# Kernel tuning notes

Measured on AMD Instinct MI355X. Metric: run time of the kernel, lower is better.

## Reference

```python
import jax, jax.numpy as jnp
import numpy as np

B, S, D, H, DH, DK = 2, 2048, 1024, 16, 64, 64


def setup_inputs() -> dict:
    key = jax.random.key(0)
    ks = jax.random.split(key, 11)
    scale_in = 1.0 / np.sqrt(D)
    return {
        "Q": jax.random.normal(ks[0], (B, S, D), jnp.float32),
        "K": jax.random.normal(ks[1], (B, S, D), jnp.float32),
        "V": jax.random.normal(ks[2], (B, S, D), jnp.float32),
        "Wq": jax.random.normal(ks[3], (H, D, DH), jnp.float32) * scale_in,
        "bq": jax.random.normal(ks[4], (H, DH), jnp.float32) * 0.02,
        "Wk": jax.random.normal(ks[5], (H, D, DH), jnp.float32) * scale_in,
        "bk": jax.random.normal(ks[6], (H, DH), jnp.float32) * 0.02,
        "Wv": jax.random.normal(ks[7], (H, D, DH), jnp.float32) * scale_in,
        "bv": jax.random.normal(ks[8], (H, DH), jnp.float32) * 0.02,
        "Wf": jax.random.normal(ks[9], (D, D), jnp.float32) * scale_in,
        "bf": jax.random.normal(ks[10], (D,), jnp.float32) * 0.02,
    }


def reference(Q, K, V, Wq, bq, Wk, bk, Wv, bv, Wf, bf):
    # Per-head projections, vectorized over the head axis h. [B,H,S,DH]
    Qh = jnp.einsum("bsd,hde->bhse", Q, Wq) + bq[None, :, None, :]
    Kh = jnp.einsum("bsd,hde->bhse", K, Wk) + bk[None, :, None, :]
    Vh = jnp.einsum("bsd,hde->bhse", V, Wv) + bv[None, :, None, :]
    inv_sqrt_dk = jnp.asarray(1.0 / np.sqrt(DK), Qh.dtype)
    # Full attention matrix [B,H,S,S] (faithful to the naive original).
    scores = jnp.einsum("bhse,bhte->bhst", Qh, Kh) * inv_sqrt_dk
    attn = jax.nn.softmax(scores, axis=-1)  # F.softmax default -> last dim
    out = jnp.einsum("bhst,bhte->bhse", attn, Vh)  # [B,H,S,DH]
    # Concat heads on the feature axis: [B,S,H*DH] == [B,S,D]
    out = out.transpose(0, 2, 1, 3).reshape(Q.shape[0], Q.shape[1], -1)
    return out @ Wf + bf
```

## Files before the change

### kernel.cpp

```cpp
#include <hip/hip_runtime.h>

#define DEV __device__ __forceinline__

typedef unsigned short u16;
typedef unsigned int   u32;
typedef __attribute__((ext_vector_type(4)))  float f32x4;
typedef __attribute__((ext_vector_type(8)))  short s16x8;
typedef __attribute__((ext_vector_type(2)))  u32   u32x2;

static constexpr size_t OFF_QBF  = 0;
static constexpr size_t OFF_KBF  = 8388608;
static constexpr size_t OFF_VBF  = 16777216;
static constexpr size_t OFF_WCAT = 25165824;
static constexpr size_t OFF_WFT  = 31457280;
static constexpr size_t OFF_BIAS = 33554432;
static constexpr size_t OFF_QKVH = 33566720;
static constexpr size_t OFF_VT   = 58732544;
static constexpr size_t OFF_OBUF = 67121152;

DEV u16 f2bf(float f) {
  union { float f; u32 u; } a; a.f = f;
  u32 r = a.u + 0x7FFFu + ((a.u >> 16) & 1u);
  return (u16)(r >> 16);
}

#if __has_builtin(__builtin_amdgcn_exp2f)
DEV float fast_exp2(float x) { return __builtin_amdgcn_exp2f(x); }
#else
DEV float fast_exp2(float x) { return exp2f(x); }
#endif

DEV f32x4 mfma16(s16x8 a, s16x8 b, f32x4 c) {
  return __builtin_amdgcn_mfma_f32_16x16x32_bf16(a, b, c, 0, 0, 0);
}

DEV void gload_lds16(const void* g, void* l) {
  __builtin_amdgcn_global_load_lds(
      (__attribute__((address_space(1))) void*)g,
      (__attribute__((address_space(3))) void*)l, 16, 0, 0);
}


__global__ __launch_bounds__(256) void cvt3_k(const float* __restrict__ Q,
                                              const float* __restrict__ K,
                                              const float* __restrict__ V,
                                              u16* __restrict__ dst) {
  size_t idx = (size_t)blockIdx.x * 256 + threadIdx.x;
  size_t t   = idx >> 20;
  size_t r   = idx & 1048575;
  const float* src = (t == 0) ? Q : (t == 1) ? K : V;
  f32x4 v = *(const f32x4*)(src + r * 4);
  u32x2 o;
  o[0] = (u32)f2bf(v[0]) | ((u32)f2bf(v[1]) << 16);
  o[1] = (u32)f2bf(v[2]) | ((u32)f2bf(v[3]) << 16);
  *(u32x2*)(dst + idx * 4) = o;
}

__global__ __launch_bounds__(256) void prep_wqkv_k(const float* __restrict__ Wq,
                                                   const float* __restrict__ Wk,
                                                   const float* __restrict__ Wv,
                                                   u16* __restrict__ Wcat) {
  const int dt = blockIdx.x, h = blockIdx.y, z = blockIdx.z;
  const float* W = (z == 0) ? Wq : (z == 1) ? Wk : Wv;
  __shared__ u16 t[64][65];
#pragma unroll
  for (int p = 0; p < 16; ++p) {
    int idx = threadIdx.x + p * 256;
    int r = idx >> 6, e = idx & 63;
    t[r][e] = f2bf(W[((size_t)h * 1024 + dt * 64 + r) * 64 + e]);
  }
  __syncthreads();
#pragma unroll
  for (int p = 0; p < 16; ++p) {
    int idx = threadIdx.x + p * 256;
    int e = idx >> 6, r = idx & 63;
    Wcat[((size_t)z * 1024 + h * 64 + e) * 1024 + dt * 64 + r] = t[r][e];
  }
}

__global__ __launch_bounds__(256) void prep_wf_k(const float* __restrict__ Wf,
                                                 u16* __restrict__ WfT) {
  const int dt = blockIdx.x, ft = blockIdx.y;
  __shared__ u16 t[64][65];
#pragma unroll
  for (int p = 0; p < 16; ++p) {
    int idx = threadIdx.x + p * 256;
    int r = idx >> 6, f = idx & 63;
    t[r][f] = f2bf(Wf[(size_t)(dt * 64 + r) * 1024 + ft * 64 + f]);
  }
  __syncthreads();
#pragma unroll
  for (int p = 0; p < 16; ++p) {
    int idx = threadIdx.x + p * 256;
    int f = idx >> 6, r = idx & 63;
    WfT[(size_t)(ft * 64 + f) * 1024 + dt * 64 + r] = t[r][f];
  }
}

__global__ __launch_bounds__(256) void prep_bias_k(const float* __restrict__ bq,
                                                   const float* __restrict__ bk,
                                                   const float* __restrict__ bv,
                                                   float* __restrict__ biascat) {
  int i = blockIdx.x * 256 + threadIdx.x;
  if (i < 1024) biascat[i] = bq[i];
  else if (i < 2048) biascat[i] = bk[i - 1024];
  else if (i < 3072) biascat[i] = bv[i - 2048];
}

__global__ __launch_bounds__(256) void transpose_vh_k(const u16* __restrict__ QKVh,
                                                      u16* __restrict__ Vt) {
  const int nt = blockIdx.x, mt = blockIdx.y;
  __shared__ u16 t[64][72];
#pragma unroll
  for (int p = 0; p < 16; ++p) {
    int idx = threadIdx.x + p * 256;
    int r = idx >> 6, c = idx & 63;
    t[r][c] = QKVh[(size_t)(mt * 64 + r) * 3072 + 2048 + nt * 64 + c];
  }
  __syncthreads();
#pragma unroll
  for (int p = 0; p < 16; ++p) {
    int idx = threadIdx.x + p * 256;
    int c = idx >> 6, r = idx & 63;
    Vt[(size_t)(nt * 64 + c) * 4096 + mt * 64 + r] = t[r][c];
  }
}

template <int BF16_OUT>
DEV void gemm128(const u16* __restrict__ A, int lda,
                 const u16* __restrict__ B, int ldb,
                 const float* __restrict__ bias,
                 void* __restrict__ Cp, size_t ldc, int K) {
  __shared__ u16 Ash[128 * 32];
  __shared__ u16 Bsh[128 * 32];
  const int tid = threadIdx.x;
  const int lane = tid & 63;
  const int w = tid >> 6;
  const int wr = w >> 1, wc = w & 1;
  const int lr = lane >> 2;
  const int lc = (lane & 3) << 3;
  const int l15 = lane & 15, lg = lane >> 4;

  f32x4 acc[4][4];
#pragma unroll
  for (int i = 0; i < 4; ++i)
#pragma unroll
    for (int j = 0; j < 4; ++j) acc[i][j] = f32x4{0.f, 0.f, 0.f, 0.f};

  for (int kt = 0; kt < K; kt += 32) {
    if (kt) __syncthreads();
#pragma unroll
    for (int j = 0; j < 2; ++j) {
      const u16* ga = A + (size_t)(w * 32 + j * 16 + lr) * lda + kt + lc;
      gload_lds16(ga, (char*)Ash + (w * 2 + j) * 1024);
      const u16* gb = B + (size_t)(w * 32 + j * 16 + lr) * ldb + kt + lc;
      gload_lds16(gb, (char*)Bsh + (w * 2 + j) * 1024);
    }
    __syncthreads();
    s16x8 af[4], bv_[4];
#pragma unroll
    for (int i = 0; i < 4; ++i) {
      af[i]  = *(const s16x8*)&Ash[(wr * 64 + i * 16 + l15) * 32 + lg * 8];
      bv_[i] = *(const s16x8*)&Bsh[(wc * 64 + i * 16 + l15) * 32 + lg * 8];
    }
#pragma unroll
    for (int mf = 0; mf < 4; ++mf)
#pragma unroll
      for (int nf = 0; nf < 4; ++nf)
        acc[mf][nf] = mfma16(af[mf], bv_[nf], acc[mf][nf]);
  }
#pragma unroll
  for (int nf = 0; nf < 4; ++nf) {
    const int nn = wc * 64 + nf * 16 + l15;
    const float bvv = bias[nn];
#pragma unroll
    for (int mf = 0; mf < 4; ++mf)
#pragma unroll
      for (int j = 0; j < 4; ++j) {
        const int mm = wr * 64 + mf * 16 + lg * 4 + j;
        float v = acc[mf][nf][j] + bvv;
        if (BF16_OUT) ((u16*)Cp)[(size_t)mm * ldc + nn] = f2bf(v);
        else          ((float*)Cp)[(size_t)mm * ldc + nn] = v;
      }
  }
}

__global__ __launch_bounds__(256) void proj_gemm_k(const u16* __restrict__ Qb,
                                                   const u16* __restrict__ Kb,
                                                   const u16* __restrict__ Vb,
                                                   const u16* __restrict__ Wcat,
                                                   const float* __restrict__ biascat,
                                                   u16* __restrict__ QKVh) {
  const int z = blockIdx.z;
  const u16* A = (z == 0) ? Qb : (z == 1) ? Kb : Vb;
  const int m0 = blockIdx.y * 128;
  const int nl = blockIdx.x * 128;
  gemm128<1>(A + (size_t)m0 * 1024, 1024,
             Wcat + (size_t)(z * 1024 + nl) * 1024, 1024,
             biascat + z * 1024 + nl,
             QKVh + (size_t)m0 * 3072 + z * 1024 + nl, 3072, 1024);
}

__global__ __launch_bounds__(256) void final_gemm_k(const u16* __restrict__ Obuf,
                                                    const u16* __restrict__ WfT,
                                                    const float* __restrict__ bf,
                                                    float* __restrict__ out) {
  const int m0 = blockIdx.y * 128;
  const int n0 = blockIdx.x * 128;
  gemm128<0>(Obuf + (size_t)m0 * 1024, 1024,
             WfT + (size_t)n0 * 1024, 1024,
             bf + n0,
             out + (size_t)m0 * 1024 + n0, 1024, 1024);
}

__global__ __launch_bounds__(256) void attn4_k(const u16* __restrict__ QKVh,
                                               const u16* __restrict__ Vt,
                                               u16* __restrict__ Obuf) {
  const int id = blockIdx.x;
  const int virt = (id & 7) * 64 + (id >> 3);
  const int qb = virt & 15;
  const int hb = virt >> 4;
  const int h = hb & 15, b = hb >> 4;

  const int tid = threadIdx.x, lane = tid & 63, w = tid >> 6;
  const int l15 = lane & 15, lg = lane >> 4;

  __shared__ u16 Ksh[64 * 64];
  __shared__ u16 Vsh[64 * 64];
  __shared__ u16 Psh[4][32 * 64];

  const size_t rowQ = (size_t)(b * 2048 + qb * 128);
  const u16* Qbase = QKVh + rowQ * 3072 + h * 64;
  const u16* Kbase = QKVh + (size_t)(b * 2048) * 3072 + 1024 + h * 64;
  const u16* Vbase = Vt + (size_t)(h * 64) * 4096 + b * 2048;

  s16x8 aq[2][2];
#pragma unroll
  for (int mf = 0; mf < 2; ++mf)
#pragma unroll
    for (int kf = 0; kf < 2; ++kf)
      aq[mf][kf] = *(const s16x8*)(Qbase + (size_t)(w * 32 + mf * 16 + l15) * 3072 + kf * 32 + lg * 8);

  f32x4 accO[2][4];
  f32x4 lacc[2];
#pragma unroll
  for (int mf = 0; mf < 2; ++mf) {
#pragma unroll
    for (int nf = 0; nf < 4; ++nf) accO[mf][nf] = f32x4{0.f, 0.f, 0.f, 0.f};
    lacc[mf] = f32x4{0.f, 0.f, 0.f, 0.f};
  }

  const float CSC = 0.18033688011112042f;
  const float M2 = 12.0f;
  const s16x8 ONESV = {0x3F80, 0x3F80, 0x3F80, 0x3F80,
                       0x3F80, 0x3F80, 0x3F80, 0x3F80};

  const int sr = tid >> 3, ch = tid & 7;
  const int sswz = (sr & 7) << 4;
  const u16* Kg = Kbase + (size_t)sr * 3072 + ch * 8;
  const u16* Vg = Vbase + (size_t)sr * 4096 + ch * 8;

  s16x8 kreg0 = *(const s16x8*)Kg;
  s16x8 kreg1 = *(const s16x8*)(Kg + (size_t)32 * 3072);
  s16x8 vreg0 = *(const s16x8*)Vg;
  s16x8 vreg1 = *(const s16x8*)(Vg + (size_t)32 * 4096);
  Kg += (size_t)64 * 3072;
  Vg += 64;

  for (int kt = 0; kt < 32; ++kt) {
    if (kt) __syncthreads();
    *(s16x8*)((char*)Ksh + sr * 128 + ((ch * 16) ^ sswz)) = kreg0;
    *(s16x8*)((char*)Ksh + (sr + 32) * 128 + ((ch * 16) ^ sswz)) = kreg1;
    *(s16x8*)((char*)Vsh + sr * 128 + ((ch * 16) ^ sswz)) = vreg0;
    *(s16x8*)((char*)Vsh + (sr + 32) * 128 + ((ch * 16) ^ sswz)) = vreg1;
    __syncthreads();

    if (kt < 31) {
      kreg0 = *(const s16x8*)Kg;
      kreg1 = *(const s16x8*)(Kg + (size_t)32 * 3072);
      vreg0 = *(const s16x8*)Vg;
      vreg1 = *(const s16x8*)(Vg + (size_t)32 * 4096);
      Kg += (size_t)64 * 3072;
      Vg += 64;
    }

    f32x4 sc[2][4];
#pragma unroll
    for (int mf = 0; mf < 2; ++mf)
#pragma unroll
      for (int nf = 0; nf < 4; ++nf) sc[mf][nf] = f32x4{0.f, 0.f, 0.f, 0.f};
#pragma unroll
    for (int kf = 0; kf < 2; ++kf) {
      s16x8 kb[4];
#pragma unroll
      for (int nf = 0; nf < 4; ++nf) {
        int row = nf * 16 + l15;
        kb[nf] = *(const s16x8*)((char*)Ksh + row * 128 + ((kf * 64 + lg * 16) ^ ((row & 7) << 4)));
      }
#pragma unroll
      for (int mf = 0; mf < 2; ++mf)
#pragma unroll
        for (int nf = 0; nf < 4; ++nf)
          sc[mf][nf] = mfma16(aq[mf][kf], kb[nf], sc[mf][nf]);
    }

#pragma unroll
    for (int mf = 0; mf < 2; ++mf)
#pragma unroll
      for (int nf = 0; nf < 4; ++nf)
#pragma unroll
        for (int j = 0; j < 4; ++j)
          sc[mf][nf][j] = fast_exp2(fmaf(sc[mf][nf][j], CSC, -M2));

    char* pbase = (char*)&Psh[w][0];
#pragma unroll
    for (int mf = 0; mf < 2; ++mf)
#pragma unroll
      for (int nf = 0; nf < 4; ++nf)
#pragma unroll
        for (int j = 0; j < 4; ++j) {
          int srow = mf * 16 + lg * 4 + j;
          int tcol = nf * 16 + l15;
          *(u16*)(pbase + srow * 128 + ((tcol * 2) ^ ((srow & 7) << 4))) =
              f2bf(sc[mf][nf][j]);
        }
    asm volatile("s_waitcnt lgkmcnt(0)" ::: "memory");

#pragma unroll
    for (int kf = 0; kf < 2; ++kf) {
      s16x8 pa[2], vb[4];
#pragma unroll
      for (int mf = 0; mf < 2; ++mf) {
        int row = mf * 16 + l15;
        pa[mf] = *(const s16x8*)(pbase + row * 128 + ((kf * 64 + lg * 16) ^ ((row & 7) << 4)));
      }
#pragma unroll
      for (int nf = 0; nf < 4; ++nf) {
        int row = nf * 16 + l15;
        vb[nf] = *(const s16x8*)((char*)Vsh + row * 128 + ((kf * 64 + lg * 16) ^ ((row & 7) << 4)));
      }
#pragma unroll
      for (int mf = 0; mf < 2; ++mf) {
#pragma unroll
        for (int nf = 0; nf < 4; ++nf)
          accO[mf][nf] = mfma16(pa[mf], vb[nf], accO[mf][nf]);
        lacc[mf] = mfma16(pa[mf], ONESV, lacc[mf]);
      }
    }
  }

  u16* Ob = Obuf + rowQ * 1024 + h * 64;
  float inv[2][4];
#pragma unroll
  for (int mf = 0; mf < 2; ++mf)
#pragma unroll
    for (int j = 0; j < 4; ++j) inv[mf][j] = 1.f / lacc[mf][j];
#pragma unroll
  for (int mf = 0; mf < 2; ++mf)
#pragma unroll
    for (int nf = 0; nf < 4; ++nf)
#pragma unroll
      for (int j = 0; j < 4; ++j)
        Ob[(size_t)(w * 32 + mf * 16 + lg * 4 + j) * 1024 + nf * 16 + l15] =
            f2bf(accO[mf][nf][j] * inv[mf][j]);
}

extern "C" void kernel_launch(void* const* d_in, const int* in_sizes, int n_in,
                              void* d_out, int out_size, void* d_ws, size_t ws_size,
                              hipStream_t stream) {
  const float* Q  = (const float*)d_in[0];
  const float* K  = (const float*)d_in[1];
  const float* V  = (const float*)d_in[2];
  const float* Wq = (const float*)d_in[3];
  const float* bq = (const float*)d_in[4];
  const float* Wk = (const float*)d_in[5];
  const float* bk = (const float*)d_in[6];
  const float* Wv = (const float*)d_in[7];
  const float* bv = (const float*)d_in[8];
  const float* Wf = (const float*)d_in[9];
  const float* bf = (const float*)d_in[10];
  float* out = (float*)d_out;
  char* ws = (char*)d_ws;

  u16*   Qbf    = (u16*)(ws + OFF_QBF);
  u16*   Kbf    = (u16*)(ws + OFF_KBF);
  u16*   Vbf    = (u16*)(ws + OFF_VBF);
  u16*   Wcat   = (u16*)(ws + OFF_WCAT);
  u16*   WfT    = (u16*)(ws + OFF_WFT);
  float* biascat= (float*)(ws + OFF_BIAS);
  u16*   QKVh   = (u16*)(ws + OFF_QKVH);
  u16*   Vt     = (u16*)(ws + OFF_VT);
  u16*   Obuf   = (u16*)(ws + OFF_OBUF);

  dim3 blk(256);
  cvt3_k<<<12288, blk, 0, stream>>>(Q, K, V, Qbf);
  prep_wqkv_k<<<dim3(16, 16, 3), blk, 0, stream>>>(Wq, Wk, Wv, Wcat);
  prep_wf_k<<<dim3(16, 16), blk, 0, stream>>>(Wf, WfT);
  prep_bias_k<<<12, blk, 0, stream>>>(bq, bk, bv, biascat);
  proj_gemm_k<<<dim3(8, 32, 3), blk, 0, stream>>>(Qbf, Kbf, Vbf, Wcat, biascat, QKVh);
  transpose_vh_k<<<dim3(16, 64), blk, 0, stream>>>(QKVh, Vt);
  attn4_k<<<dim3(512), blk, 0, stream>>>(QKVh, Vt, Obuf);
  final_gemm_k<<<dim3(8, 32), blk, 0, stream>>>(Obuf, WfT, bf, out);
}
```

Baseline: 148.5 us.

## Load K/V MFMA fragments directly from global memory, dropping LDS staging and barriers

The attention kernel no longer stages K and V tiles through shared memory with block-wide barriers. Each wave now loads its MFMA operand fragments for K and V straight from global memory, relying on L1/L2 because all four waves read the same tiles. K fragments are double-buffered in registers across iterations. Launch bounds now request two blocks per CU. This removes the syncthreads and LDS traffic but quadruples global/L2 load requests and raises register pressure.

```diff
diff --git a/kernel.cpp b/kernel.cpp
--- a/kernel.cpp
+++ b/kernel.cpp
@@ -213,9 +213,9 @@
              out + (size_t)m0 * 1024 + n0, 1024, 1024);
 }
 
-__global__ __launch_bounds__(256) void attn4_k(const u16* __restrict__ QKVh,
-                                               const u16* __restrict__ Vt,
-                                               u16* __restrict__ Obuf) {
+__global__ __launch_bounds__(256, 2) void attn5_k(const u16* __restrict__ QKVh,
+                                                  const u16* __restrict__ Vt,
+                                                  u16* __restrict__ Obuf) {
   const int id = blockIdx.x;
   const int virt = (id & 7) * 64 + (id >> 3);
   const int qb = virt & 15;
@@ -225,8 +225,6 @@
   const int tid = threadIdx.x, lane = tid & 63, w = tid >> 6;
   const int l15 = lane & 15, lg = lane >> 4;
 
-  __shared__ u16 Ksh[64 * 64];
-  __shared__ u16 Vsh[64 * 64];
   __shared__ u16 Psh[4][32 * 64];
 
   const size_t rowQ = (size_t)(b * 2048 + qb * 128);
@@ -255,34 +253,26 @@
   const s16x8 ONESV = {0x3F80, 0x3F80, 0x3F80, 0x3F80,
                        0x3F80, 0x3F80, 0x3F80, 0x3F80};
 
-  const int sr = tid >> 3, ch = tid & 7;
-  const int sswz = (sr & 7) << 4;
-  const u16* Kg = Kbase + (size_t)sr * 3072 + ch * 8;
-  const u16* Vg = Vbase + (size_t)sr * 4096 + ch * 8;
-
-  s16x8 kreg0 = *(const s16x8*)Kg;
-  s16x8 kreg1 = *(const s16x8*)(Kg + (size_t)32 * 3072);
-  s16x8 vreg0 = *(const s16x8*)Vg;
-  s16x8 vreg1 = *(const s16x8*)(Vg + (size_t)32 * 4096);
-  Kg += (size_t)64 * 3072;
-  Vg += 64;
-
-  for (int kt = 0; kt < 32; ++kt) {
-    if (kt) __syncthreads();
-    *(s16x8*)((char*)Ksh + sr * 128 + ((ch * 16) ^ sswz)) = kreg0;
-    *(s16x8*)((char*)Ksh + (sr + 32) * 128 + ((ch * 16) ^ sswz)) = kreg1;
-    *(s16x8*)((char*)Vsh + sr * 128 + ((ch * 16) ^ sswz)) = vreg0;
-    *(s16x8*)((char*)Vsh + (sr + 32) * 128 + ((ch * 16) ^ sswz)) = vreg1;
-    __syncthreads();
-
-    if (kt < 31) {
-      kreg0 = *(const s16x8*)Kg;
-      kreg1 = *(const s16x8*)(Kg + (size_t)32 * 3072);
-      vreg0 = *(const s16x8*)Vg;
-      vreg1 = *(const s16x8*)(Vg + (size_t)32 * 4096);
-      Kg += (size_t)64 * 3072;
-      Vg += 64;
-    }
+  const u16* Kf = Kbase + (size_t)l15 * 3072 + lg * 8;
+  const u16* Vf = Vbase + (size_t)l15 * 4096 + lg * 8;
+  char* pbase = (char*)&Psh[w][0];
+
+  auto LOADK = [&](s16x8 (&dst)[2][4], int t) {
+#pragma unroll
+    for (int kf = 0; kf < 2; ++kf)
+#pragma unroll
+      for (int nf = 0; nf < 4; ++nf)
+        dst[kf][nf] = *(const s16x8*)(Kf + (size_t)(t * 64 + nf * 16) * 3072 + kf * 32);
+  };
+
+  auto TILE = [&](s16x8 (&kcur)[2][4], s16x8 (&knext)[2][4], int kt) {
+    if (kt + 1 < 32) LOADK(knext, kt + 1);
+    s16x8 vb[2][4];
+#pragma unroll
+    for (int kf = 0; kf < 2; ++kf)
+#pragma unroll
+      for (int nf = 0; nf < 4; ++nf)
+        vb[kf][nf] = *(const s16x8*)(Vf + (size_t)(nf * 16) * 4096 + kt * 64 + kf * 32);
 
     f32x4 sc[2][4];
 #pragma unroll
@@ -290,19 +280,12 @@
 #pragma unroll
       for (int nf = 0; nf < 4; ++nf) sc[mf][nf] = f32x4{0.f, 0.f, 0.f, 0.f};
 #pragma unroll
-    for (int kf = 0; kf < 2; ++kf) {
-      s16x8 kb[4];
-#pragma unroll
-      for (int nf = 0; nf < 4; ++nf) {
-        int row = nf * 16 + l15;
-        kb[nf] = *(const s16x8*)((char*)Ksh + row * 128 + ((kf * 64 + lg * 16) ^ ((row & 7) << 4)));
-      }
+    for (int kf = 0; kf < 2; ++kf)
 #pragma unroll
       for (int mf = 0; mf < 2; ++mf)
 #pragma unroll
         for (int nf = 0; nf < 4; ++nf)
-          sc[mf][nf] = mfma16(aq[mf][kf], kb[nf], sc[mf][nf]);
-    }
+          sc[mf][nf] = mfma16(aq[mf][kf], kcur[kf][nf], sc[mf][nf]);
 
 #pragma unroll
     for (int mf = 0; mf < 2; ++mf)
@@ -312,7 +295,6 @@
         for (int j = 0; j < 4; ++j)
           sc[mf][nf][j] = fast_exp2(fmaf(sc[mf][nf][j], CSC, -M2));
 
-    char* pbase = (char*)&Psh[w][0];
 #pragma unroll
     for (int mf = 0; mf < 2; ++mf)
 #pragma unroll
@@ -328,25 +310,27 @@
 
 #pragma unroll
     for (int kf = 0; kf < 2; ++kf) {
-      s16x8 pa[2], vb[4];
+      s16x8 pa[2];
 #pragma unroll
       for (int mf = 0; mf < 2; ++mf) {
         int row = mf * 16 + l15;
         pa[mf] = *(const s16x8*)(pbase + row * 128 + ((kf * 64 + lg * 16) ^ ((row & 7) << 4)));
       }
 #pragma unroll
-      for (int nf = 0; nf < 4; ++nf) {
-        int row = nf * 16 + l15;
-        vb[nf] = *(const s16x8*)((char*)Vsh + row * 128 + ((kf * 64 + lg * 16) ^ ((row & 7) << 4)));
-      }
-#pragma unroll
       for (int mf = 0; mf < 2; ++mf) {
 #pragma unroll
         for (int nf = 0; nf < 4; ++nf)
-          accO[mf][nf] = mfma16(pa[mf], vb[nf], accO[mf][nf]);
+          accO[mf][nf] = mfma16(pa[mf], vb[kf][nf], accO[mf][nf]);
         lacc[mf] = mfma16(pa[mf], ONESV, lacc[mf]);
       }
     }
+  };
+
+  s16x8 kbufA[2][4], kbufB[2][4];
+  LOADK(kbufA, 0);
+  for (int kt = 0; kt < 32; kt += 2) {
+    TILE(kbufA, kbufB, kt);
+    TILE(kbufB, kbufA, kt + 1);
   }
 
   u16* Ob = Obuf + rowQ * 1024 + h * 64;
@@ -399,6 +383,6 @@
   prep_bias_k<<<12, blk, 0, stream>>>(bq, bk, bv, biascat);
   proj_gemm_k<<<dim3(8, 32, 3), blk, 0, stream>>>(Qbf, Kbf, Vbf, Wcat, biascat, QKVh);
   transpose_vh_k<<<dim3(16, 64), blk, 0, stream>>>(QKVh, Vt);
-  attn4_k<<<dim3(512), blk, 0, stream>>>(QKVh, Vt, Obuf);
+  attn5_k<<<dim3(512), blk, 0, stream>>>(QKVh, Vt, Obuf);
   final_gemm_k<<<dim3(8, 32), blk, 0, stream>>>(Obuf, WfT, bf, out);
 }
```

New measurement: 209.1 us. 1.41x slower.

## Merge prep kernels into one launch and write V projection transposed

Applied to the files above, without the earlier changes.

Four preprocessing kernels (input bf16 conversion, QKV weight transpose, Wf transpose, bias concat) are merged into one launch that branches on block index. The V projection GEMM now writes its bf16 output directly in transposed layout, with packed 8-byte stores, so the separate transpose kernel and its extra pass over V are gone. A sched_barrier is added in the attention kernel after the P store wait. Together these cut launch overhead and memory traffic, but the transposed store pattern may coalesce less well than the row-major stores.

```diff
diff --git a/kernel.cpp b/kernel.cpp
--- a/kernel.cpp
+++ b/kernel.cpp
@@ -23,6 +23,9 @@
   u32 r = a.u + 0x7FFFu + ((a.u >> 16) & 1u);
   return (u16)(r >> 16);
 }
+DEV u32 f2bf2(float lo, float hi_) {
+  return (u32)f2bf(lo) | ((u32)f2bf(hi_) << 16);
+}
 
 #if __has_builtin(__builtin_amdgcn_exp2f)
 DEV float fast_exp2(float x) { return __builtin_amdgcn_exp2f(x); }
@@ -40,93 +43,74 @@
       (__attribute__((address_space(3))) void*)l, 16, 0, 0);
 }
 
-
-__global__ __launch_bounds__(256) void cvt3_k(const float* __restrict__ Q,
-                                              const float* __restrict__ K,
-                                              const float* __restrict__ V,
-                                              u16* __restrict__ dst) {
-  size_t idx = (size_t)blockIdx.x * 256 + threadIdx.x;
-  size_t t   = idx >> 20;
-  size_t r   = idx & 1048575;
-  const float* src = (t == 0) ? Q : (t == 1) ? K : V;
-  f32x4 v = *(const f32x4*)(src + r * 4);
-  u32x2 o;
-  o[0] = (u32)f2bf(v[0]) | ((u32)f2bf(v[1]) << 16);
-  o[1] = (u32)f2bf(v[2]) | ((u32)f2bf(v[3]) << 16);
-  *(u32x2*)(dst + idx * 4) = o;
-}
-
-__global__ __launch_bounds__(256) void prep_wqkv_k(const float* __restrict__ Wq,
-                                                   const float* __restrict__ Wk,
-                                                   const float* __restrict__ Wv,
-                                                   u16* __restrict__ Wcat) {
-  const int dt = blockIdx.x, h = blockIdx.y, z = blockIdx.z;
-  const float* W = (z == 0) ? Wq : (z == 1) ? Wk : Wv;
-  __shared__ u16 t[64][65];
-#pragma unroll
-  for (int p = 0; p < 16; ++p) {
-    int idx = threadIdx.x + p * 256;
-    int r = idx >> 6, e = idx & 63;
-    t[r][e] = f2bf(W[((size_t)h * 1024 + dt * 64 + r) * 64 + e]);
-  }
-  __syncthreads();
-#pragma unroll
-  for (int p = 0; p < 16; ++p) {
-    int idx = threadIdx.x + p * 256;
-    int e = idx >> 6, r = idx & 63;
-    Wcat[((size_t)z * 1024 + h * 64 + e) * 1024 + dt * 64 + r] = t[r][e];
-  }
-}
-
-__global__ __launch_bounds__(256) void prep_wf_k(const float* __restrict__ Wf,
-                                                 u16* __restrict__ WfT) {
-  const int dt = blockIdx.x, ft = blockIdx.y;
-  __shared__ u16 t[64][65];
-#pragma unroll
-  for (int p = 0; p < 16; ++p) {
-    int idx = threadIdx.x + p * 256;
-    int r = idx >> 6, f = idx & 63;
-    t[r][f] = f2bf(Wf[(size_t)(dt * 64 + r) * 1024 + ft * 64 + f]);
-  }
-  __syncthreads();
-#pragma unroll
-  for (int p = 0; p < 16; ++p) {
-    int idx = threadIdx.x + p * 256;
-    int f = idx >> 6, r = idx & 63;
-    WfT[(size_t)(ft * 64 + f) * 1024 + dt * 64 + r] = t[r][f];
-  }
-}
-
-__global__ __launch_bounds__(256) void prep_bias_k(const float* __restrict__ bq,
-                                                   const float* __restrict__ bk,
-                                                   const float* __restrict__ bv,
-                                                   float* __restrict__ biascat) {
-  int i = blockIdx.x * 256 + threadIdx.x;
-  if (i < 1024) biascat[i] = bq[i];
-  else if (i < 2048) biascat[i] = bk[i - 1024];
-  else if (i < 3072) biascat[i] = bv[i - 2048];
-}
-
-__global__ __launch_bounds__(256) void transpose_vh_k(const u16* __restrict__ QKVh,
-                                                      u16* __restrict__ Vt) {
-  const int nt = blockIdx.x, mt = blockIdx.y;
+__global__ __launch_bounds__(256) void prep_all_k(const float* __restrict__ Q,
+                                                  const float* __restrict__ K,
+                                                  const float* __restrict__ V,
+                                                  const float* __restrict__ Wq,
+                                                  const float* __restrict__ Wk,
+                                                  const float* __restrict__ Wv,
+                                                  const float* __restrict__ Wf,
+                                                  const float* __restrict__ bq,
+                                                  const float* __restrict__ bk,
+                                                  const float* __restrict__ bv,
+                                                  u16* __restrict__ QKVbf,
+                                                  u16* __restrict__ Wcat,
+                                                  u16* __restrict__ WfT,
+                                                  float* __restrict__ biascat) {
+  const int bid = blockIdx.x;
   __shared__ u16 t[64][72];
-#pragma unroll
-  for (int p = 0; p < 16; ++p) {
-    int idx = threadIdx.x + p * 256;
-    int r = idx >> 6, c = idx & 63;
-    t[r][c] = QKVh[(size_t)(mt * 64 + r) * 3072 + 2048 + nt * 64 + c];
-  }
-  __syncthreads();
-#pragma unroll
-  for (int p = 0; p < 16; ++p) {
-    int idx = threadIdx.x + p * 256;
-    int c = idx >> 6, r = idx & 63;
-    Vt[(size_t)(nt * 64 + c) * 4096 + mt * 64 + r] = t[r][c];
-  }
-}
-
-template <int BF16_OUT>
+  if (bid < 12288) {
+    size_t idx = (size_t)bid * 256 + threadIdx.x;
+    size_t tt  = idx >> 20;
+    size_t r   = idx & 1048575;
+    const float* src = (tt == 0) ? Q : (tt == 1) ? K : V;
+    f32x4 v = *(const f32x4*)(src + r * 4);
+    u32x2 o;
+    o[0] = f2bf2(v[0], v[1]);
+    o[1] = f2bf2(v[2], v[3]);
+    *(u32x2*)(QKVbf + idx * 4) = o;
+  } else if (bid < 13056) {
+    const int q = bid - 12288;
+    const int dt = q & 15, h = (q >> 4) & 15, z = q >> 8;
+    const float* W = (z == 0) ? Wq : (z == 1) ? Wk : Wv;
+#pragma unroll
+    for (int p = 0; p < 16; ++p) {
+      int idx = threadIdx.x + p * 256;
+      int r = idx >> 6, e = idx & 63;
+      t[r][e] = f2bf(W[((size_t)h * 1024 + dt * 64 + r) * 64 + e]);
+    }
+    __syncthreads();
+#pragma unroll
+    for (int p = 0; p < 16; ++p) {
+      int idx = threadIdx.x + p * 256;
+      int e = idx >> 6, r = idx & 63;
+      Wcat[((size_t)z * 1024 + h * 64 + e) * 1024 + dt * 64 + r] = t[r][e];
+    }
+  } else if (bid < 13312) {
+    const int q = bid - 13056;
+    const int dt = q & 15, ft = q >> 4;
+#pragma unroll
+    for (int p = 0; p < 16; ++p) {
+      int idx = threadIdx.x + p * 256;
+      int r = idx >> 6, f = idx & 63;
+      t[r][f] = f2bf(Wf[(size_t)(dt * 64 + r) * 1024 + ft * 64 + f]);
+    }
+    __syncthreads();
+#pragma unroll
+    for (int p = 0; p < 16; ++p) {
+      int idx = threadIdx.x + p * 256;
+      int f = idx >> 6, r = idx & 63;
+      WfT[(size_t)(ft * 64 + f) * 1024 + dt * 64 + r] = t[r][f];
+    }
+  } else {
+    int i = (bid - 13312) * 256 + threadIdx.x;
+    if (i < 1024) biascat[i] = bq[i];
+    else if (i < 2048) biascat[i] = bk[i - 1024];
+    else if (i < 3072) biascat[i] = bv[i - 2048];
+  }
+}
+
+template <int MODE>
 DEV void gemm128(const u16* __restrict__ A, int lda,
                  const u16* __restrict__ B, int ldb,
                  const float* __restrict__ bias,
@@ -174,14 +158,23 @@
     const int nn = wc * 64 + nf * 16 + l15;
     const float bvv = bias[nn];
 #pragma unroll
-    for (int mf = 0; mf < 4; ++mf)
-#pragma unroll
-      for (int j = 0; j < 4; ++j) {
-        const int mm = wr * 64 + mf * 16 + lg * 4 + j;
-        float v = acc[mf][nf][j] + bvv;
-        if (BF16_OUT) ((u16*)Cp)[(size_t)mm * ldc + nn] = f2bf(v);
-        else          ((float*)Cp)[(size_t)mm * ldc + nn] = v;
+    for (int mf = 0; mf < 4; ++mf) {
+      if (MODE == 2) {
+        const int mm0 = wr * 64 + mf * 16 + lg * 4;
+        u32x2 d;
+        d[0] = f2bf2(acc[mf][nf][0] + bvv, acc[mf][nf][1] + bvv);
+        d[1] = f2bf2(acc[mf][nf][2] + bvv, acc[mf][nf][3] + bvv);
+        *(u32x2*)((u16*)Cp + (size_t)nn * ldc + mm0) = d;
+      } else {
+#pragma unroll
+        for (int j = 0; j < 4; ++j) {
+          const int mm = wr * 64 + mf * 16 + lg * 4 + j;
+          float v = acc[mf][nf][j] + bvv;
+          if (MODE == 1) ((u16*)Cp)[(size_t)mm * ldc + nn] = f2bf(v);
+          else           ((float*)Cp)[(size_t)mm * ldc + nn] = v;
+        }
       }
+    }
   }
 }
 
@@ -190,15 +183,23 @@
                                                    const u16* __restrict__ Vb,
                                                    const u16* __restrict__ Wcat,
                                                    const float* __restrict__ biascat,
-                                                   u16* __restrict__ QKVh) {
+                                                   u16* __restrict__ QKVh,
+                                                   u16* __restrict__ Vt) {
   const int z = blockIdx.z;
   const u16* A = (z == 0) ? Qb : (z == 1) ? Kb : Vb;
   const int m0 = blockIdx.y * 128;
   const int nl = blockIdx.x * 128;
-  gemm128<1>(A + (size_t)m0 * 1024, 1024,
-             Wcat + (size_t)(z * 1024 + nl) * 1024, 1024,
-             biascat + z * 1024 + nl,
-             QKVh + (size_t)m0 * 3072 + z * 1024 + nl, 3072, 1024);
+  if (z == 2) {
+    gemm128<2>(A + (size_t)m0 * 1024, 1024,
+               Wcat + (size_t)(2 * 1024 + nl) * 1024, 1024,
+               biascat + 2 * 1024 + nl,
+               Vt + (size_t)nl * 4096 + m0, 4096, 1024);
+  } else {
+    gemm128<1>(A + (size_t)m0 * 1024, 1024,
+               Wcat + (size_t)(z * 1024 + nl) * 1024, 1024,
+               biascat + z * 1024 + nl,
+               QKVh + (size_t)m0 * 3072 + z * 1024 + nl, 3072, 1024);
+  }
 }
 
 __global__ __launch_bounds__(256) void final_gemm_k(const u16* __restrict__ Obuf,
@@ -213,7 +214,7 @@
              out + (size_t)m0 * 1024 + n0, 1024, 1024);
 }
 
-__global__ __launch_bounds__(256) void attn4_k(const u16* __restrict__ QKVh,
+__global__ __launch_bounds__(256) void attn7_k(const u16* __restrict__ QKVh,
                                                const u16* __restrict__ Vt,
                                                u16* __restrict__ Obuf) {
   const int id = blockIdx.x;
@@ -325,6 +326,7 @@
               f2bf(sc[mf][nf][j]);
         }
     asm volatile("s_waitcnt lgkmcnt(0)" ::: "memory");
+    __builtin_amdgcn_sched_barrier(0);
 
 #pragma unroll
     for (int kf = 0; kf < 2; ++kf) {
@@ -382,6 +384,7 @@
   float* out = (float*)d_out;
   char* ws = (char*)d_ws;
 
+  u16*   QKVbf  = (u16*)(ws + OFF_QBF);
   u16*   Qbf    = (u16*)(ws + OFF_QBF);
   u16*   Kbf    = (u16*)(ws + OFF_KBF);
   u16*   Vbf    = (u16*)(ws + OFF_VBF);
@@ -393,12 +396,10 @@
   u16*   Obuf   = (u16*)(ws + OFF_OBUF);
 
   dim3 blk(256);
-  cvt3_k<<<12288, blk, 0, stream>>>(Q, K, V, Qbf);
-  prep_wqkv_k<<<dim3(16, 16, 3), blk, 0, stream>>>(Wq, Wk, Wv, Wcat);
-  prep_wf_k<<<dim3(16, 16), blk, 0, stream>>>(Wf, WfT);
-  prep_bias_k<<<12, blk, 0, stream>>>(bq, bk, bv, biascat);
-  proj_gemm_k<<<dim3(8, 32, 3), blk, 0, stream>>>(Qbf, Kbf, Vbf, Wcat, biascat, QKVh);
-  transpose_vh_k<<<dim3(16, 64), blk, 0, stream>>>(QKVh, Vt);
-  attn4_k<<<dim3(512), blk, 0, stream>>>(QKVh, Vt, Obuf);
+  prep_all_k<<<13324, blk, 0, stream>>>(Q, K, V, Wq, Wk, Wv, Wf, bq, bk, bv,
+                                        QKVbf, Wcat, WfT, biascat);
+  proj_gemm_k<<<dim3(8, 32, 3), blk, 0, stream>>>(Qbf, Kbf, Vbf, Wcat, biascat,
+                                                  QKVh, Vt);
+  attn7_k<<<dim3(512), blk, 0, stream>>>(QKVh, Vt, Obuf);
   final_gemm_k<<<dim3(8, 32), blk, 0, stream>>>(Obuf, WfT, bf, out);
 }
```

After: 139.8 us. 1.06x faster.
